# Optimization experiments

Measured on AMD Instinct MI355X. Metric: run time of the kernel, lower is better.

## Reference

```python
import jax, jax.numpy as jnp
import numpy as np

B, LIN, DIN, D, NQ, H, NB, DI, DS, K, DTR = 4, 2048, 512, 1024, 256, 16, 4, 2048, 16, 4, 64


def _ln(x, g, b, eps=1e-5):
    m = x.mean(-1, keepdims=True)
    v = ((x - m) ** 2).mean(-1, keepdims=True)
    return (x - m) * jax.lax.rsqrt(v + eps) * g + b


def setup_inputs() -> dict:
    key = jax.random.key(0)
    ks = iter(jax.random.split(key, 40))
    r = lambda *s: jax.random.normal(next(ks), s, jnp.float32) * 0.02
    inp = dict(
        x=jax.random.normal(next(ks), (B, LIN, DIN), jnp.float32),
        mask=jnp.ones((B, LIN), bool),
        W_in=r(D, DIN), b_in=jnp.zeros((D,), jnp.float32),
        latents=r(1, NQ, D),
        lnq_g=jnp.ones((D,), jnp.float32), lnq_b=jnp.zeros((D,), jnp.float32),
        lnkv_g=jnp.ones((D,), jnp.float32), lnkv_b=jnp.zeros((D,), jnp.float32),
        W_qkv=r(3 * D, D), b_qkv=jnp.zeros((3 * D,), jnp.float32),
        W_o=r(D, D), b_o=jnp.zeros((D,), jnp.float32),
        W1=r(2 * D, D), b1=jnp.zeros((2 * D,), jnp.float32),
        W2=r(D, 2 * D), b2=jnp.zeros((D,), jnp.float32),
        lnf_g=jnp.ones((D,), jnp.float32), lnf_b=jnp.zeros((D,), jnp.float32),
        mb_ln_g=jnp.ones((NB, D), jnp.float32), mb_ln_b=jnp.zeros((NB, D), jnp.float32),
        mb_Win=r(NB, 2 * DI, D),
        mb_conv_w=r(NB, DI, K), mb_conv_b=jnp.zeros((NB, DI), jnp.float32),
        mb_xproj=r(NB, DTR + 2 * DS, DI),
        mb_dtW=r(NB, DI, DTR), mb_dtb=r(NB, DI),
        mb_Alog=jnp.log(jnp.broadcast_to(jnp.arange(1, DS + 1, dtype=jnp.float32), (NB, DI, DS))),
        mb_D=jnp.ones((NB, DI), jnp.float32),
        mb_Wout=r(NB, D, DI),
        enc_ln_g=jnp.ones((D,), jnp.float32), enc_ln_b=jnp.zeros((D,), jnp.float32),
        out_ln_g=jnp.ones((D,), jnp.float32), out_ln_b=jnp.zeros((D,), jnp.float32),
    )
    return inp


def _mamba(u, Win, cw, cb, xp, dtW, dtb, Alog, Dp, Wout):
    # u: [B, NQ, D]
    xz = u @ Win.T                              # [B, NQ, 2*DI]
    xin, z = jnp.split(xz, 2, axis=-1)
    # causal depthwise conv1d over time
    xc = jax.lax.conv_general_dilated(
        xin.transpose(0, 2, 1), cw[:, None, :], (1,), [(K - 1, 0)],
        feature_group_count=DI)                 # [B, DI, NQ]
    xc = jax.nn.silu((xc + cb[None, :, None]).transpose(0, 2, 1))  # [B, NQ, DI]
    dbl = xc @ xp.T                             # [B, NQ, DTR + 2*DS]
    dtr = dbl[..., :DTR]
    Bm = dbl[..., DTR:DTR + DS]
    Cm = dbl[..., DTR + DS:]
    delta = jax.nn.softplus(dtr @ dtW.T + dtb)  # [B, NQ, DI]
    A = -jnp.exp(Alog)                          # [DI, DS]

    def step(h, inputs):
        dt, bt, ct, xt = inputs                 # dt,xt: [B,DI]; bt,ct: [B,DS]
        h = jnp.exp(dt[..., None] * A) * h + (dt * xt)[..., None] * bt[:, None, :]
        return h, jnp.einsum('bdn,bn->bd', h, ct)

    xs = (delta.transpose(1, 0, 2), Bm.transpose(1, 0, 2),
          Cm.transpose(1, 0, 2), xc.transpose(1, 0, 2))
    h0 = jnp.zeros((u.shape[0], DI, DS), u.dtype)
    _, ys = jax.lax.scan(step, h0, xs)          # ys: [NQ, B, DI]
    y = ys.transpose(1, 0, 2) + Dp * xc
    return (y * jax.nn.silu(z)) @ Wout.T


def reference(x, mask, W_in, b_in, latents, lnq_g, lnq_b, lnkv_g, lnkv_b,
              W_qkv, b_qkv, W_o, b_o, W1, b1, W2, b2, lnf_g, lnf_b,
              mb_ln_g, mb_ln_b, mb_Win, mb_conv_w, mb_conv_b, mb_xproj,
              mb_dtW, mb_dtb, mb_Alog, mb_D, mb_Wout,
              enc_ln_g, enc_ln_b, out_ln_g, out_ln_b):
    bsz = x.shape[0]
    h = x @ W_in.T + b_in                               # [B, LIN, D]
    q = _ln(jnp.broadcast_to(latents, (bsz, NQ, D)), lnq_g, lnq_b)
    kv = _ln(h, lnkv_g, lnkv_b)
    Wq, Wk, Wv = jnp.split(W_qkv, 3, 0)
    bq, bk, bv = jnp.split(b_qkv, 3, 0)
    hd = D // H
    qh = (q @ Wq.T + bq).reshape(bsz, NQ, H, hd)
    kh = (kv @ Wk.T + bk).reshape(bsz, LIN, H, hd)
    vh = (kv @ Wv.T + bv).reshape(bsz, LIN, H, hd)
    sc = jnp.einsum('bqhd,bkhd->bhqk', qh, kh) / jnp.float32(np.sqrt(hd))
    sc = jnp.where(mask[:, None, None, :], sc, jnp.float32(-1e9))
    attn = jax.nn.softmax(sc, axis=-1)
    o = jnp.einsum('bhqk,bkhd->bqhd', attn, vh).reshape(bsz, NQ, D) @ W_o.T + b_o
    hq = q + o
    ff = jax.nn.gelu(hq @ W1.T + b1, approximate=False) @ W2.T + b2
    hq = _ln(hq + ff, lnf_g, lnf_b)
    for i in range(mb_ln_g.shape[0]):
        hq = hq + _mamba(_ln(hq, mb_ln_g[i], mb_ln_b[i]), mb_Win[i],
                         mb_conv_w[i], mb_conv_b[i], mb_xproj[i], mb_dtW[i],
                         mb_dtb[i], mb_Alog[i], mb_D[i], mb_Wout[i])
    hq = _ln(hq, enc_ln_g, enc_ln_b)
    out = _ln(hq, out_ln_g, out_ln_b)
    comp_mask = jnp.ones((bsz, NQ), bool)
    return (out, comp_mask)
```

## Files before the change

kernel.cpp:

```cpp
#include <hip/hip_runtime.h>
#include <hip/hip_bf16.h>
#include <math.h>

typedef __attribute__((ext_vector_type(8))) short s16x8;
typedef __attribute__((ext_vector_type(4))) float f32x4;

static __device__ __forceinline__ unsigned short f2bf(float f) {
    unsigned u = __builtin_bit_cast(unsigned, f);
    u += 0x7fffu + ((u >> 16) & 1u);
    return (unsigned short)(u >> 16);
}

static __device__ __forceinline__ void gload16(const void* g, void* l) {
    __builtin_amdgcn_global_load_lds(
        (const __attribute__((address_space(1))) unsigned int*)g,
        (__attribute__((address_space(3))) unsigned int*)l, 16, 0, 0);
}

template<int ACT, bool ACC, bool BIAS, int OUT>
__global__ __launch_bounds__(256)
void gemm_bf16(const unsigned short* __restrict__ A, const unsigned short* __restrict__ B,
               const float* __restrict__ bias, float* __restrict__ Cf,
               unsigned short* __restrict__ Cb,
               int M, int N, int K, int lda, int ldb, int ldc)
{
    __shared__ alignas(16) unsigned short As[128][32];
    __shared__ alignas(16) unsigned short Bs[128][32];

    const int tid = threadIdx.x;
    const int m0 = blockIdx.y * 128;
    const int n0 = blockIdx.x * 128;
    const int l  = tid & 63;
    const int w  = tid >> 6;
    const int wr = w >> 1, wc = w & 1;
    const int fr = l & 15;
    const int fk = (l >> 4) * 8;
    const int srow = l >> 2;
    const int skel = (l & 3) * 8;

    f32x4 acc[4][4];
#pragma unroll
    for (int i = 0; i < 4; ++i)
#pragma unroll
        for (int j = 0; j < 4; ++j) acc[i][j] = (f32x4){0.f, 0.f, 0.f, 0.f};

    for (int k0 = 0; k0 < K; k0 += 32) {
#pragma unroll
        for (int c = 0; c < 2; ++c) {
            const int r0 = w * 32 + c * 16;
            gload16(A + (size_t)(m0 + r0 + srow) * lda + k0 + skel, &As[r0][0]);
            gload16(B + (size_t)(n0 + r0 + srow) * ldb + k0 + skel, &Bs[r0][0]);
        }
        __syncthreads();

        s16x8 af[4], bfg[4];
#pragma unroll
        for (int mi = 0; mi < 4; ++mi)
            af[mi] = *reinterpret_cast<const s16x8*>(&As[wr * 64 + mi * 16 + fr][fk]);
#pragma unroll
        for (int ni = 0; ni < 4; ++ni)
            bfg[ni] = *reinterpret_cast<const s16x8*>(&Bs[wc * 64 + ni * 16 + fr][fk]);
#pragma unroll
        for (int mi = 0; mi < 4; ++mi)
#pragma unroll
            for (int ni = 0; ni < 4; ++ni)
                acc[mi][ni] = __builtin_amdgcn_mfma_f32_16x16x32_bf16(
                    af[mi], bfg[ni], acc[mi][ni], 0, 0, 0);
        __syncthreads();
    }

#pragma unroll
    for (int mi = 0; mi < 4; ++mi) {
#pragma unroll
        for (int ni = 0; ni < 4; ++ni) {
            const int col = n0 + wc * 64 + ni * 16 + fr;
            float bs = BIAS ? bias[col] : 0.f;
            f32x4 v = acc[mi][ni];
#pragma unroll
            for (int r = 0; r < 4; ++r) {
                const int row = m0 + wr * 64 + mi * 16 + (l >> 4) * 4 + r;
                float val = v[r] + bs;
                if (ACT == 1) val = 0.5f * val * (1.0f + erff(val * 0.70710678118654752440f));
                size_t idx = (size_t)row * ldc + col;
                if (OUT == 0) {
                    if (ACC) val += Cf[idx];
                    Cf[idx] = val;
                } else {
                    Cb[idx] = f2bf(val);
                }
            }
        }
    }
}

template<int ACT, bool ACC, bool BIAS, int OUT>
__global__ __launch_bounds__(256)
void gemm_bf16_t64(const unsigned short* __restrict__ A, const unsigned short* __restrict__ B,
                   const float* __restrict__ bias, float* __restrict__ Cf,
                   unsigned short* __restrict__ Cb,
                   int M, int N, int K, int lda, int ldb, int ldc)
{
    __shared__ alignas(16) unsigned short As[64][32];
    __shared__ alignas(16) unsigned short Bs[64][32];

    const int tid = threadIdx.x;
    const int m0 = blockIdx.y * 64;
    const int n0 = blockIdx.x * 64;
    const int l  = tid & 63;
    const int w  = tid >> 6;
    const int wr = w >> 1, wc = w & 1;
    const int fr = l & 15;
    const int fk = (l >> 4) * 8;

    f32x4 acc[2][2];
#pragma unroll
    for (int i = 0; i < 2; ++i)
#pragma unroll
        for (int j = 0; j < 2; ++j) acc[i][j] = (f32x4){0.f, 0.f, 0.f, 0.f};

    for (int k0 = 0; k0 < K; k0 += 32) {
        gload16(A + (size_t)(m0 + w * 16 + (l >> 2)) * lda + k0 + (l & 3) * 8, &As[w * 16][0]);
        gload16(B + (size_t)(n0 + w * 16 + (l >> 2)) * ldb + k0 + (l & 3) * 8, &Bs[w * 16][0]);
        __syncthreads();

        s16x8 af[2], bfg[2];
#pragma unroll
        for (int mi = 0; mi < 2; ++mi)
            af[mi] = *reinterpret_cast<const s16x8*>(&As[wr * 32 + mi * 16 + fr][fk]);
#pragma unroll
        for (int ni = 0; ni < 2; ++ni)
            bfg[ni] = *reinterpret_cast<const s16x8*>(&Bs[wc * 32 + ni * 16 + fr][fk]);
#pragma unroll
        for (int mi = 0; mi < 2; ++mi)
#pragma unroll
            for (int ni = 0; ni < 2; ++ni)
                acc[mi][ni] = __builtin_amdgcn_mfma_f32_16x16x32_bf16(
                    af[mi], bfg[ni], acc[mi][ni], 0, 0, 0);
        __syncthreads();
    }

#pragma unroll
    for (int mi = 0; mi < 2; ++mi) {
#pragma unroll
        for (int ni = 0; ni < 2; ++ni) {
            const int col = n0 + wc * 32 + ni * 16 + fr;
            float bs = BIAS ? bias[col] : 0.f;
            f32x4 v = acc[mi][ni];
#pragma unroll
            for (int r = 0; r < 4; ++r) {
                const int row = m0 + wr * 32 + mi * 16 + (l >> 4) * 4 + r;
                float val = v[r] + bs;
                if (ACT == 1) val = 0.5f * val * (1.0f + erff(val * 0.70710678118654752440f));
                size_t idx = (size_t)row * ldc + col;
                if (OUT == 0) {
                    if (ACC) val += Cf[idx];
                    Cf[idx] = val;
                } else {
                    Cb[idx] = f2bf(val);
                }
            }
        }
    }
}

template<int ACT, bool BIAS, bool ATOMIC>
__global__ __launch_bounds__(256)
void gemm_bt(const float* __restrict__ A, const float* __restrict__ B,
             const float* __restrict__ bias, float* __restrict__ C,
             int M, int N, int K, int lda, int ldb, int ldc, int ksplit)
{
    __shared__ alignas(16) float As[16][68];
    __shared__ alignas(16) float Bs[16][68];
    const int tid = threadIdx.x;
    const int m0 = blockIdx.y * 64;
    const int n0 = blockIdx.x * 64;
    const int ty = tid >> 4, tx = tid & 15;
    const int lrow = tid >> 2;
    const int lk   = (tid & 3) << 2;

    float acc[4][4] = {};
    const int kbeg = blockIdx.z * ksplit;
    const int kend = kbeg + ksplit;

    for (int k0 = kbeg; k0 < kend; k0 += 16) {
        {
            int gr = m0 + lrow;
            float4 v; v.x = v.y = v.z = v.w = 0.f;
            if (gr < M) v = *reinterpret_cast<const float4*>(A + (size_t)gr * lda + k0 + lk);
            As[lk + 0][lrow] = v.x; As[lk + 1][lrow] = v.y;
            As[lk + 2][lrow] = v.z; As[lk + 3][lrow] = v.w;
        }
        {
            int gr = n0 + lrow;
            float4 v; v.x = v.y = v.z = v.w = 0.f;
            if (gr < N) v = *reinterpret_cast<const float4*>(B + (size_t)gr * ldb + k0 + lk);
            Bs[lk + 0][lrow] = v.x; Bs[lk + 1][lrow] = v.y;
            Bs[lk + 2][lrow] = v.z; Bs[lk + 3][lrow] = v.w;
        }
        __syncthreads();
#pragma unroll
        for (int k = 0; k < 16; ++k) {
            float4 a = *reinterpret_cast<const float4*>(&As[k][ty << 2]);
            float4 b = *reinterpret_cast<const float4*>(&Bs[k][tx << 2]);
            acc[0][0] += a.x * b.x; acc[0][1] += a.x * b.y; acc[0][2] += a.x * b.z; acc[0][3] += a.x * b.w;
            acc[1][0] += a.y * b.x; acc[1][1] += a.y * b.y; acc[1][2] += a.y * b.z; acc[1][3] += a.y * b.w;
            acc[2][0] += a.z * b.x; acc[2][1] += a.z * b.y; acc[2][2] += a.z * b.z; acc[2][3] += a.z * b.w;
            acc[3][0] += a.w * b.x; acc[3][1] += a.w * b.y; acc[3][2] += a.w * b.z; acc[3][3] += a.w * b.w;
        }
        __syncthreads();
    }

#pragma unroll
    for (int i = 0; i < 4; ++i) {
        int m = m0 + (ty << 2) + i;
        if (m >= M) continue;
#pragma unroll
        for (int j = 0; j < 4; ++j) {
            int n = n0 + (tx << 2) + j;
            if (n >= N) continue;
            float v = acc[i][j];
            if (BIAS && blockIdx.z == 0) v += bias[n];
            if (ACT == 2) v = fmaxf(v, 0.f) + log1pf(expf(-fabsf(v)));
            size_t idx = (size_t)m * ldc + n;
            if (ATOMIC) atomicAdd(&C[idx], v);
            else C[idx] = v;
        }
    }
}

template<bool RES, int OUT>
__global__ __launch_bounds__(256)
void ln_k(const float* __restrict__ x, const float* __restrict__ res,
          const float* __restrict__ g, const float* __restrict__ b,
          float* __restrict__ outf, unsigned short* __restrict__ outb)
{
    int row = blockIdx.x;
    int t = threadIdx.x;
    float4 v = reinterpret_cast<const float4*>(x + (size_t)row * 1024)[t];
    if (RES) {
        float4 r2 = reinterpret_cast<const float4*>(res + (size_t)row * 1024)[t];
        v.x += r2.x; v.y += r2.y; v.z += r2.z; v.w += r2.w;
    }
    float s  = v.x + v.y + v.z + v.w;
    float ss = v.x * v.x + v.y * v.y + v.z * v.z + v.w * v.w;
#pragma unroll
    for (int off = 32; off > 0; off >>= 1) {
        s  += __shfl_down(s, off, 64);
        ss += __shfl_down(ss, off, 64);
    }
    __shared__ float red[2][4];
    __shared__ float mv[2];
    int wid = t >> 6;
    if ((t & 63) == 0) { red[0][wid] = s; red[1][wid] = ss; }
    __syncthreads();
    if (t == 0) {
        float S  = red[0][0] + red[0][1] + red[0][2] + red[0][3];
        float SS = red[1][0] + red[1][1] + red[1][2] + red[1][3];
        float mean = S * (1.f / 1024.f);
        float var  = SS * (1.f / 1024.f) - mean * mean;
        mv[0] = mean; mv[1] = rsqrtf(var + 1e-5f);
    }
    __syncthreads();
    float mean = mv[0], rstd = mv[1];
    float4 gg = reinterpret_cast<const float4*>(g)[t];
    float4 bb = reinterpret_cast<const float4*>(b)[t];
    float y0 = (v.x - mean) * rstd * gg.x + bb.x;
    float y1 = (v.y - mean) * rstd * gg.y + bb.y;
    float y2 = (v.z - mean) * rstd * gg.z + bb.z;
    float y3 = (v.w - mean) * rstd * gg.w + bb.w;
    if (OUT == 0 || OUT == 2) {
        float4 ov; ov.x = y0; ov.y = y1; ov.z = y2; ov.w = y3;
        reinterpret_cast<float4*>(outf + (size_t)row * 1024)[t] = ov;
    }
    if (OUT == 1 || OUT == 2) {
        unsigned long long p = (unsigned long long)f2bf(y0)
                             | ((unsigned long long)f2bf(y1) << 16)
                             | ((unsigned long long)f2bf(y2) << 32)
                             | ((unsigned long long)f2bf(y3) << 48);
        *reinterpret_cast<unsigned long long*>(outb + (size_t)row * 1024 + t * 4) = p;
    }
}

__global__ __launch_bounds__(256)
void attn_part_mfma(const unsigned short* __restrict__ qh,
                    const unsigned short* __restrict__ kv,
                    float* __restrict__ pacc, float* __restrict__ pml)
{
    const int bx = blockIdx.x;
    const int split = bx & 3;
    const int qsp = (bx >> 2) & 3;
    const int h = (bx >> 4) & 15;
    const int b = bx >> 8;
    const int tid = threadIdx.x;
    const int l = tid & 63, w = tid >> 6;
    const int g = l >> 4, q4 = l & 15;

    __shared__ alignas(16) unsigned short Ks[64][72];
    __shared__ alignas(16) unsigned short Vt[64][72];
    __shared__ alignas(16) unsigned short Ps[4][64][20];

    s16x8 qf[2];
    {
        const int qrow = qsp * 64 + w * 16 + q4;
        const unsigned short* qp = qh + (size_t)qrow * 1024 + h * 64 + g * 8;
        qf[0] = *reinterpret_cast<const s16x8*>(qp);
        qf[1] = *reinterpret_cast<const s16x8*>(qp + 32);
    }

    f32x4 oacc[4];
#pragma unroll
    for (int mi = 0; mi < 4; ++mi) oacc[mi] = (f32x4){0.f, 0.f, 0.f, 0.f};
    float m_run = -1e30f, l_run = 0.f;

    const unsigned short* khb = kv + ((size_t)b * 2048 + split * 512) * 2048 + h * 64;
    const unsigned short* vhb = khb + 1024;

    const int krow = tid >> 2, dcol = (tid & 3) << 4;

    for (int kt = 0; kt < 512; kt += 64) {
        __syncthreads();
        {
            const unsigned short* ksrc = khb + (size_t)(kt + krow) * 2048 + dcol;
            s16x8 k0 = *reinterpret_cast<const s16x8*>(ksrc);
            s16x8 k1 = *reinterpret_cast<const s16x8*>(ksrc + 8);
            *reinterpret_cast<s16x8*>(&Ks[krow][dcol]) = k0;
            *reinterpret_cast<s16x8*>(&Ks[krow][dcol + 8]) = k1;
            const unsigned short* vsrc = vhb + (size_t)(kt + krow) * 2048 + dcol;
            s16x8 v0 = *reinterpret_cast<const s16x8*>(vsrc);
            s16x8 v1 = *reinterpret_cast<const s16x8*>(vsrc + 8);
            const int kb = krow >> 3, klo = krow & 7;
#pragma unroll
            for (int ii = 0; ii < 8; ++ii) {
                int d0 = dcol + ii, d1 = dcol + 8 + ii;
                Vt[d0][((kb ^ ((d0 >> 3) & 7)) << 3) + klo] = (unsigned short)v0[ii];
                Vt[d1][((kb ^ ((d1 >> 3) & 7)) << 3) + klo] = (unsigned short)v1[ii];
            }
        }
        __syncthreads();

        f32x4 sacc[4];
#pragma unroll
        for (int mt = 0; mt < 4; ++mt) sacc[mt] = (f32x4){0.f, 0.f, 0.f, 0.f};
#pragma unroll
        for (int dc = 0; dc < 2; ++dc) {
#pragma unroll
            for (int mt = 0; mt < 4; ++mt) {
                s16x8 ka = *reinterpret_cast<const s16x8*>(&Ks[mt * 16 + q4][g * 8 + dc * 32]);
                sacc[mt] = __builtin_amdgcn_mfma_f32_16x16x32_bf16(ka, qf[dc], sacc[mt], 0, 0, 0);
            }
        }

        float p[16];
        float pmax = -1e30f;
#pragma unroll
        for (int mt = 0; mt < 4; ++mt)
#pragma unroll
            for (int r = 0; r < 4; ++r)
                pmax = fmaxf(pmax, sacc[mt][r] * 0.125f);
        pmax = fmaxf(pmax, __shfl_xor(pmax, 16));
        pmax = fmaxf(pmax, __shfl_xor(pmax, 32));
        float m_new = fmaxf(m_run, pmax);
        float sc_o = __expf(m_run - m_new);
        float lpart = 0.f;
#pragma unroll
        for (int mt = 0; mt < 4; ++mt)
#pragma unroll
            for (int r = 0; r < 4; ++r) {
                float pv = __expf(sacc[mt][r] * 0.125f - m_new);
                p[mt * 4 + r] = pv;
                lpart += pv;
            }
        lpart += __shfl_xor(lpart, 16);
        lpart += __shfl_xor(lpart, 32);
        l_run = l_run * sc_o + lpart;
        m_run = m_new;
#pragma unroll
        for (int mi = 0; mi < 4; ++mi)
#pragma unroll
            for (int r = 0; r < 4; ++r)
                oacc[mi][r] *= sc_o;

#pragma unroll
        for (int mt = 0; mt < 4; ++mt)
#pragma unroll
            for (int r = 0; r < 4; ++r)
                Ps[w][mt * 16 + g * 4 + r][q4] = f2bf(p[mt * 4 + r]);

#pragma unroll
        for (int kc = 0; kc < 2; ++kc) {
            s16x8 pb;
#pragma unroll
            for (int j = 0; j < 8; ++j)
                pb[j] = (short)Ps[w][kc * 32 + g * 8 + j][q4];
#pragma unroll
            for (int mi = 0; mi < 4; ++mi) {
                const int d = mi * 16 + q4;
                s16x8 va = *reinterpret_cast<const s16x8*>(
                    &Vt[d][((4 * kc + g) ^ ((d >> 3) & 7)) << 3]);
                oacc[mi] = __builtin_amdgcn_mfma_f32_16x16x32_bf16(va, pb, oacc[mi], 0, 0, 0);
            }
        }
    }

    const int rowg = (b * 16 + h) * 256 + qsp * 64 + w * 16 + q4;
    float* pa = pacc + ((size_t)split * 16384 + rowg) * 64;
#pragma unroll
    for (int mi = 0; mi < 4; ++mi)
        *reinterpret_cast<f32x4*>(pa + mi * 16 + g * 4) = oacc[mi];
    if (g == 0) {
        pml[((size_t)split * 16384 + rowg) * 2 + 0] = m_run;
        pml[((size_t)split * 16384 + rowg) * 2 + 1] = l_run;
    }
}

__global__ __launch_bounds__(64)
void attn_comb_k(const float* __restrict__ pacc, const float* __restrict__ pml,
                 unsigned short* __restrict__ o)
{
    int row = blockIdx.x * 64 + threadIdx.x;
    float M = -1e30f;
#pragma unroll
    for (int s = 0; s < 4; ++s)
        M = fmaxf(M, pml[((size_t)s * 16384 + row) * 2]);
    float L = 0.f;
    float out[64] = {};
#pragma unroll
    for (int s = 0; s < 4; ++s) {
        float ms = pml[((size_t)s * 16384 + row) * 2 + 0];
        float ls = pml[((size_t)s * 16384 + row) * 2 + 1];
        float wgt = __expf(ms - M);
        L += wgt * ls;
        const float4* ap = reinterpret_cast<const float4*>(pacc + ((size_t)s * 16384 + row) * 64);
#pragma unroll
        for (int d4 = 0; d4 < 16; ++d4) {
            float4 a = ap[d4];
            out[d4 * 4 + 0] += wgt * a.x; out[d4 * 4 + 1] += wgt * a.y;
            out[d4 * 4 + 2] += wgt * a.z; out[d4 * 4 + 3] += wgt * a.w;
        }
    }
    float inv = 1.f / L;
    int t = row & 63, qt = (row >> 6) & 3, h = (row >> 8) & 15, b = row >> 12;
    unsigned short* op = o + (size_t)(b * 256 + qt * 64 + t) * 1024 + h * 64;
#pragma unroll
    for (int d8 = 0; d8 < 8; ++d8) {
        s16x8 v;
#pragma unroll
        for (int j = 0; j < 8; ++j) v[j] = (short)f2bf(out[d8 * 8 + j] * inv);
        *reinterpret_cast<s16x8*>(op + d8 * 8) = v;
    }
}

__global__ void add_bcast_k(const float* __restrict__ q, const float* __restrict__ o,
                            float* __restrict__ hq, unsigned short* __restrict__ hqb)
{
    int i = blockIdx.x * 256 + threadIdx.x;
    int r = i >> 8, c = i & 255;
    float4 qv = reinterpret_cast<const float4*>(q)[(r & 255) * 256 + c];
    float4 ov = reinterpret_cast<const float4*>(o)[i];
    float4 s; s.x = qv.x + ov.x; s.y = qv.y + ov.y; s.z = qv.z + ov.z; s.w = qv.w + ov.w;
    reinterpret_cast<float4*>(hq)[i] = s;
    unsigned long long p = (unsigned long long)f2bf(s.x)
                         | ((unsigned long long)f2bf(s.y) << 16)
                         | ((unsigned long long)f2bf(s.z) << 32)
                         | ((unsigned long long)f2bf(s.w) << 48);
    *reinterpret_cast<unsigned long long*>(hqb + (size_t)r * 1024 + c * 4) = p;
}

__global__ void conv_k(const float* __restrict__ xz, const float* __restrict__ cw,
                       const float* __restrict__ cb, float* __restrict__ xc)
{
    int i = blockIdx.x * 256 + threadIdx.x;
    int r = i >> 11, c = i & 2047;
    int t = r & 255;
    float a = cb[c];
#pragma unroll
    for (int k = 0; k < 4; ++k) {
        int tt = t - 3 + k;
        if (tt >= 0) a += xz[(size_t)(r - 3 + k) * 4096 + c] * cw[c * 4 + k];
    }
    xc[i] = a / (1.f + expf(-a));
}

__global__ __launch_bounds__(256)
void scan_gate_k(const float* __restrict__ delta, const float* __restrict__ dbl,
                 const float* __restrict__ xc, const float* __restrict__ Alog,
                 const float* __restrict__ xz, const float* __restrict__ Dp,
                 unsigned short* __restrict__ gb)
{
    const int t = threadIdx.x;
    const int pi = t & 15, seg = t >> 4;
    const int pr = blockIdx.x * 16 + pi;
    const int c = pr & 2047, b = pr >> 11;

    float A[16];
#pragma unroll
    for (int n = 0; n < 16; ++n) A[n] = -expf(Alog[c * 16 + n]);
    const float Dc = Dp[c];

    __shared__ float HE[15][16][17];
    __shared__ float HU[15][16][17];

    if (seg < 15) {
        float h[16], E[16];
#pragma unroll
        for (int n = 0; n < 16; ++n) { h[n] = 0.f; E[n] = 1.f; }
        for (int s = 0; s < 16; ++s) {
            int r = b * 256 + seg * 16 + s;
            float dt = delta[(size_t)r * 2048 + c];
            float xv = xc[(size_t)r * 2048 + c];
            const float* row = dbl + (size_t)r * 96;
            float dx = dt * xv;
#pragma unroll
            for (int n = 0; n < 16; ++n) {
                float e = __expf(dt * A[n]);
                h[n] = e * h[n] + dx * row[64 + n];
                E[n] *= e;
            }
        }
#pragma unroll
        for (int n = 0; n < 16; ++n) { HE[seg][pi][n] = E[n]; HU[seg][pi][n] = h[n]; }
    }
    __syncthreads();

    float hs[16];
#pragma unroll
    for (int n = 0; n < 16; ++n) hs[n] = 0.f;
    for (int s2 = 0; s2 < seg; ++s2) {
#pragma unroll
        for (int n = 0; n < 16; ++n)
            hs[n] = HE[s2][pi][n] * hs[n] + HU[s2][pi][n];
    }

    for (int s = 0; s < 16; ++s) {
        int r = b * 256 + seg * 16 + s;
        float dt = delta[(size_t)r * 2048 + c];
        float xv = xc[(size_t)r * 2048 + c];
        const float* row = dbl + (size_t)r * 96;
        float dx = dt * xv;
        float y = 0.f;
#pragma unroll
        for (int n = 0; n < 16; ++n) {
            float e = __expf(dt * A[n]);
            hs[n] = e * hs[n] + dx * row[64 + n];
            y += hs[n] * row[80 + n];
        }
        float zv = xz[(size_t)r * 4096 + 2048 + c];
        float gv = (y + Dc * xv) * (zv / (1.f + expf(-zv)));
        gb[(size_t)r * 2048 + c] = f2bf(gv);
    }
}

__global__ __launch_bounds__(256)
void cvt_bf16_k(const float* __restrict__ in, unsigned short* __restrict__ out)
{
    size_t i = ((size_t)blockIdx.x * 256 + threadIdx.x) * 8;
    float4 a = *reinterpret_cast<const float4*>(in + i);
    float4 b = *reinterpret_cast<const float4*>(in + i + 4);
    s16x8 v;
    v[0] = (short)f2bf(a.x); v[1] = (short)f2bf(a.y);
    v[2] = (short)f2bf(a.z); v[3] = (short)f2bf(a.w);
    v[4] = (short)f2bf(b.x); v[5] = (short)f2bf(b.y);
    v[6] = (short)f2bf(b.z); v[7] = (short)f2bf(b.w);
    *reinterpret_cast<s16x8*>(out + i) = v;
}

__global__ void fill_ones_f32(float* p, int n)
{
    int i = blockIdx.x * 256 + threadIdx.x;
    if (i < n) p[i] = 1.0f;
}

__global__ void fill_zero_f32(float* p, int n)
{
    int i = blockIdx.x * 256 + threadIdx.x;
    if (i < n) p[i] = 0.0f;
}

extern "C" void kernel_launch(void* const* d_in, const int* in_sizes, int n_in,
                              void* d_out, int out_size, void* d_ws, size_t ws_size,
                              hipStream_t stream)
{
    const float* x      = (const float*)d_in[0];
    const float* W_in   = (const float*)d_in[2];
    const float* b_in   = (const float*)d_in[3];
    const float* latents= (const float*)d_in[4];
    const float* lnq_g  = (const float*)d_in[5];
    const float* lnq_b  = (const float*)d_in[6];
    const float* lnkv_g = (const float*)d_in[7];
    const float* lnkv_b = (const float*)d_in[8];
    const float* W_qkv  = (const float*)d_in[9];
    const float* b_qkv  = (const float*)d_in[10];
    const float* W_o    = (const float*)d_in[11];
    const float* b_o    = (const float*)d_in[12];
    const float* W1     = (const float*)d_in[13];
    const float* b1     = (const float*)d_in[14];
    const float* W2     = (const float*)d_in[15];
    const float* b2     = (const float*)d_in[16];
    const float* lnf_g  = (const float*)d_in[17];
    const float* lnf_b  = (const float*)d_in[18];
    const float* mb_ln_g= (const float*)d_in[19];
    const float* mb_ln_b= (const float*)d_in[20];
    const float* mb_Win = (const float*)d_in[21];
    const float* mb_cw  = (const float*)d_in[22];
    const float* mb_cb  = (const float*)d_in[23];
    const float* mb_xp  = (const float*)d_in[24];
    const float* mb_dtW = (const float*)d_in[25];
    const float* mb_dtb = (const float*)d_in[26];
    const float* mb_Alog= (const float*)d_in[27];
    const float* mb_D   = (const float*)d_in[28];
    const float* mb_Wout= (const float*)d_in[29];
    const float* enc_g  = (const float*)d_in[30];
    const float* enc_b  = (const float*)d_in[31];
    const float* out_g  = (const float*)d_in[32];
    const float* out_b  = (const float*)d_in[33];

    float* W = (float*)d_ws;
    typedef unsigned short us;
    float* kvh  = W + 0;
    float* qln  = W + 25165824;
    float* op   = W + 26738688;
    float* hq   = W + 27787264;
    us* P       = (us*)(W + 8388608);
    us* kv_bf   = P + 0;
    us* KV      = P + 8388608;
    us* qh_bf   = P + 25165824;
    us* Wqkv_bf = P + 25427968;
    us* Win_bf  = P + 28573696;
    us* xbf     = P + 29097984;
    float* pacc = kvh;
    float* pml  = op;
    us* Wo_bf   = (us*)(W + 4194304);
    us* W1_bf   = (us*)(W + 4718592);
    us* W2_bf   = (us*)(W + 5767168);
    us* ff1_bf  = (us*)(W + 6815744);
    us* hq_bf   = (us*)(W + 7864320);
    us* o_bf    = (us*)(W + 25690112);
    us* qln_bf  = (us*)(W + 26214400);
    us* Win_all = (us*)(W + 8388608);
    us* Wout_all= (us*)(W + 16777216);
    us* u_bf    = (us*)(W + 0);
    float* xz   = W + 524288;
    float* xc   = W + 4718592;
    float* dbl  = W + 6815744;
    float* dly  = W + 20971520;
    us* gb_bf   = (us*)(W + 23068672);
    float* tmp  = W + 26214400;

    dim3 blk(256);

    cvt_bf16_k<<<2048,blk,0,stream>>>(x, xbf);
    cvt_bf16_k<<<256,blk,0,stream>>>(W_in, Win_bf);
    cvt_bf16_k<<<1536,blk,0,stream>>>(W_qkv, Wqkv_bf);
    gemm_bf16<0,false,true,0><<<dim3(8,64),blk,0,stream>>>(xbf, Win_bf, b_in, kvh, nullptr, 8192,1024,512, 512,512,1024);
    ln_k<false,1><<<8192,blk,0,stream>>>(kvh, nullptr, lnkv_g, lnkv_b, nullptr, kv_bf);
    ln_k<false,2><<<256,blk,0,stream>>>(latents, nullptr, lnq_g, lnq_b, qln, qln_bf);
    gemm_bf16_t64<0,false,true,1><<<dim3(16,4),blk,0,stream>>>(qln_bf, Wqkv_bf, b_qkv, nullptr, qh_bf, 256,1024,1024, 1024,1024,1024);
    gemm_bf16<0,false,true,1><<<dim3(16,64),blk,0,stream>>>(kv_bf, Wqkv_bf+1048576, b_qkv+1024, nullptr, KV, 8192,2048,1024, 1024,1024,2048);
    attn_part_mfma<<<1024,blk,0,stream>>>(qh_bf, KV, pacc, pml);
    cvt_bf16_k<<<512,blk,0,stream>>>(W_o, Wo_bf);
    attn_comb_k<<<256,64,0,stream>>>(pacc, pml, o_bf);
    gemm_bf16_t64<0,false,true,0><<<dim3(16,16),blk,0,stream>>>(o_bf, Wo_bf, b_o, op, nullptr, 1024,1024,1024, 1024,1024,1024);
    add_bcast_k<<<1024,blk,0,stream>>>(qln, op, hq, hq_bf);
    cvt_bf16_k<<<1024,blk,0,stream>>>(W1, W1_bf);
    cvt_bf16_k<<<1024,blk,0,stream>>>(W2, W2_bf);
    gemm_bf16_t64<1,false,true,1><<<dim3(32,16),blk,0,stream>>>(hq_bf, W1_bf, b1, nullptr, ff1_bf, 1024,2048,1024, 1024,1024,2048);
    gemm_bf16_t64<0,false,true,0><<<dim3(16,16),blk,0,stream>>>(ff1_bf, W2_bf, b2, tmp, nullptr, 1024,1024,2048, 2048,2048,1024);
    ln_k<true,0><<<1024,blk,0,stream>>>(hq, tmp, lnf_g, lnf_b, hq, nullptr);
    cvt_bf16_k<<<8192,blk,0,stream>>>(mb_Win, Win_all);
    cvt_bf16_k<<<4096,blk,0,stream>>>(mb_Wout, Wout_all);
    for (int i = 0; i < 4; ++i) {
        ln_k<false,1><<<1024,blk,0,stream>>>(hq, nullptr, mb_ln_g + i*1024, mb_ln_b + i*1024, nullptr, u_bf);
        gemm_bf16<0,false,false,0><<<dim3(32,8),blk,0,stream>>>(u_bf, Win_all + (size_t)i*4194304, nullptr, xz, nullptr, 1024,4096,1024, 1024,1024,4096);
        conv_k<<<8192,blk,0,stream>>>(xz, mb_cw + i*8192, mb_cb + i*2048, xc);
        fill_zero_f32<<<384,blk,0,stream>>>(dbl, 98304);
        gemm_bt<0,false,true><<<dim3(2,16,8),blk,0,stream>>>(xc, mb_xp + i*196608, nullptr, dbl, 1024,96,2048, 2048,2048,96, 256);
        gemm_bt<2,true,false><<<dim3(32,16,1),blk,0,stream>>>(dbl, mb_dtW + i*131072, mb_dtb + i*2048, dly, 1024,2048,64, 96,64,2048, 64);
        scan_gate_k<<<512,blk,0,stream>>>(dly, dbl, xc, mb_Alog + i*32768, xz, mb_D + i*2048, gb_bf);
        gemm_bf16_t64<0,true,false,0><<<dim3(16,16),blk,0,stream>>>(gb_bf, Wout_all + (size_t)i*2097152, nullptr, hq, nullptr, 1024,1024,2048, 2048,2048,1024);
    }
    ln_k<false,0><<<1024,blk,0,stream>>>(hq, nullptr, enc_g, enc_b, tmp, nullptr);
    ln_k<false,0><<<1024,blk,0,stream>>>(tmp, nullptr, out_g, out_b, (float*)d_out, nullptr);
    fill_ones_f32<<<4,blk,0,stream>>>((float*)d_out + 1048576, 1024);
}
```

Before: 1.015 ms.

## Add 256x256-tile GEMM for KV projection and batch weight conversions into multi-kernels

Adds a 512-thread GEMM kernel with 256x256 output tiles and a 64-wide K step, and uses it for the large 8192x2048x1024 KV projection to raise data reuse per block. It also merges eight separate fp32-to-bf16 conversion launches into two multi-segment launches, so fewer kernels are launched. The big tile uses 64KB of LDS and 128 accumulator registers per thread, with no double buffering. That can lower occupancy, and the grid has only 256 blocks.

```diff
diff --git a/kernel.cpp b/kernel.cpp
--- a/kernel.cpp
+++ b/kernel.cpp
@@ -93,6 +93,78 @@
     }
 }
 
+template<bool BIAS, int OUT>
+__global__ __launch_bounds__(512)
+void gemm_bf16_t256(const unsigned short* __restrict__ A, const unsigned short* __restrict__ B,
+                    const float* __restrict__ bias, float* __restrict__ Cf,
+                    unsigned short* __restrict__ Cb,
+                    int M, int N, int K, int lda, int ldb, int ldc)
+{
+    __shared__ alignas(16) unsigned short As[256][64];
+    __shared__ alignas(16) unsigned short Bs[256][64];
+
+    const int tid = threadIdx.x;
+    const int m0 = blockIdx.y * 256;
+    const int n0 = blockIdx.x * 256;
+    const int l  = tid & 63;
+    const int w  = tid >> 6;
+    const int wr = w >> 2, wc = w & 3;
+    const int fr = l & 15;
+    const int fk = (l >> 4) * 8;
+
+    f32x4 acc[8][4];
+#pragma unroll
+    for (int i = 0; i < 8; ++i)
+#pragma unroll
+        for (int j = 0; j < 4; ++j) acc[i][j] = (f32x4){0.f, 0.f, 0.f, 0.f};
+
+    for (int k0 = 0; k0 < K; k0 += 64) {
+#pragma unroll
+        for (int c = 0; c < 4; ++c) {
+            const int r0 = (w * 4 + c) * 8;
+            gload16(A + (size_t)(m0 + r0 + (l >> 3)) * lda + k0 + (l & 7) * 8, &As[r0][0]);
+            gload16(B + (size_t)(n0 + r0 + (l >> 3)) * ldb + k0 + (l & 7) * 8, &Bs[r0][0]);
+        }
+        __syncthreads();
+
+#pragma unroll
+        for (int kk = 0; kk < 2; ++kk) {
+            s16x8 af[8], bfg[4];
+#pragma unroll
+            for (int mi = 0; mi < 8; ++mi)
+                af[mi] = *reinterpret_cast<const s16x8*>(&As[wr * 128 + mi * 16 + fr][kk * 32 + fk]);
+#pragma unroll
+            for (int ni = 0; ni < 4; ++ni)
+                bfg[ni] = *reinterpret_cast<const s16x8*>(&Bs[wc * 64 + ni * 16 + fr][kk * 32 + fk]);
+#pragma unroll
+            for (int mi = 0; mi < 8; ++mi)
+#pragma unroll
+                for (int ni = 0; ni < 4; ++ni)
+                    acc[mi][ni] = __builtin_amdgcn_mfma_f32_16x16x32_bf16(
+                        af[mi], bfg[ni], acc[mi][ni], 0, 0, 0);
+        }
+        __syncthreads();
+    }
+
+#pragma unroll
+    for (int mi = 0; mi < 8; ++mi) {
+#pragma unroll
+        for (int ni = 0; ni < 4; ++ni) {
+            const int col = n0 + wc * 64 + ni * 16 + fr;
+            float bs = BIAS ? bias[col] : 0.f;
+            f32x4 v = acc[mi][ni];
+#pragma unroll
+            for (int r = 0; r < 4; ++r) {
+                const int row = m0 + wr * 128 + mi * 16 + (l >> 4) * 4 + r;
+                float val = v[r] + bs;
+                size_t idx = (size_t)row * ldc + col;
+                if (OUT == 0) Cf[idx] = val;
+                else          Cb[idx] = f2bf(val);
+            }
+        }
+    }
+}
+
 template<int ACT, bool ACC, bool BIAS, int OUT>
 __global__ __launch_bounds__(256)
 void gemm_bf16_t64(const unsigned short* __restrict__ A, const unsigned short* __restrict__ B,
@@ -551,17 +623,28 @@
 }
 
 __global__ __launch_bounds__(256)
-void cvt_bf16_k(const float* __restrict__ in, unsigned short* __restrict__ out)
-{
-    size_t i = ((size_t)blockIdx.x * 256 + threadIdx.x) * 8;
-    float4 a = *reinterpret_cast<const float4*>(in + i);
-    float4 b = *reinterpret_cast<const float4*>(in + i + 4);
+void cvt_multi_k(const float* s0, const float* s1, const float* s2,
+                 const float* s3, const float* s4,
+                 unsigned short* d0, unsigned short* d1, unsigned short* d2,
+                 unsigned short* d3, unsigned short* d4,
+                 int e0, int e1, int e2, int e3, int e4)
+{
+    int blk = blockIdx.x;
+    const float* s; unsigned short* d; int base;
+    if      (blk < e0) { s = s0; d = d0; base = 0;  }
+    else if (blk < e1) { s = s1; d = d1; base = e0; }
+    else if (blk < e2) { s = s2; d = d2; base = e1; }
+    else if (blk < e3) { s = s3; d = d3; base = e2; }
+    else               { s = s4; d = d4; base = e3; }
+    size_t i = ((size_t)(blk - base) * 256 + threadIdx.x) * 8;
+    float4 a = *reinterpret_cast<const float4*>(s + i);
+    float4 b = *reinterpret_cast<const float4*>(s + i + 4);
     s16x8 v;
     v[0] = (short)f2bf(a.x); v[1] = (short)f2bf(a.y);
     v[2] = (short)f2bf(a.z); v[3] = (short)f2bf(a.w);
     v[4] = (short)f2bf(b.x); v[5] = (short)f2bf(b.y);
     v[6] = (short)f2bf(b.z); v[7] = (short)f2bf(b.w);
-    *reinterpret_cast<s16x8*>(out + i) = v;
+    *reinterpret_cast<s16x8*>(d + i) = v;
 }
 
 __global__ void fill_ones_f32(float* p, int n)
@@ -648,26 +731,24 @@
 
     dim3 blk(256);
 
-    cvt_bf16_k<<<2048,blk,0,stream>>>(x, xbf);
-    cvt_bf16_k<<<256,blk,0,stream>>>(W_in, Win_bf);
-    cvt_bf16_k<<<1536,blk,0,stream>>>(W_qkv, Wqkv_bf);
+    cvt_multi_k<<<3840,blk,0,stream>>>(x, W_in, W_qkv, W_qkv, W_qkv,
+                                       xbf, Win_bf, Wqkv_bf, Wqkv_bf, Wqkv_bf,
+                                       2048, 2304, 3840, 3840, 3840);
     gemm_bf16<0,false,true,0><<<dim3(8,64),blk,0,stream>>>(xbf, Win_bf, b_in, kvh, nullptr, 8192,1024,512, 512,512,1024);
     ln_k<false,1><<<8192,blk,0,stream>>>(kvh, nullptr, lnkv_g, lnkv_b, nullptr, kv_bf);
     ln_k<false,2><<<256,blk,0,stream>>>(latents, nullptr, lnq_g, lnq_b, qln, qln_bf);
     gemm_bf16_t64<0,false,true,1><<<dim3(16,4),blk,0,stream>>>(qln_bf, Wqkv_bf, b_qkv, nullptr, qh_bf, 256,1024,1024, 1024,1024,1024);
-    gemm_bf16<0,false,true,1><<<dim3(16,64),blk,0,stream>>>(kv_bf, Wqkv_bf+1048576, b_qkv+1024, nullptr, KV, 8192,2048,1024, 1024,1024,2048);
+    gemm_bf16_t256<true,1><<<dim3(8,32),dim3(512),0,stream>>>(kv_bf, Wqkv_bf+1048576, b_qkv+1024, nullptr, KV, 8192,2048,1024, 1024,1024,2048);
     attn_part_mfma<<<1024,blk,0,stream>>>(qh_bf, KV, pacc, pml);
-    cvt_bf16_k<<<512,blk,0,stream>>>(W_o, Wo_bf);
     attn_comb_k<<<256,64,0,stream>>>(pacc, pml, o_bf);
+    cvt_multi_k<<<14848,blk,0,stream>>>(W_o, W1, W2, mb_Win, mb_Wout,
+                                        Wo_bf, W1_bf, W2_bf, Win_all, Wout_all,
+                                        512, 1536, 2560, 10752, 14848);
     gemm_bf16_t64<0,false,true,0><<<dim3(16,16),blk,0,stream>>>(o_bf, Wo_bf, b_o, op, nullptr, 1024,1024,1024, 1024,1024,1024);
     add_bcast_k<<<1024,blk,0,stream>>>(qln, op, hq, hq_bf);
-    cvt_bf16_k<<<1024,blk,0,stream>>>(W1, W1_bf);
-    cvt_bf16_k<<<1024,blk,0,stream>>>(W2, W2_bf);
     gemm_bf16_t64<1,false,true,1><<<dim3(32,16),blk,0,stream>>>(hq_bf, W1_bf, b1, nullptr, ff1_bf, 1024,2048,1024, 1024,1024,2048);
     gemm_bf16_t64<0,false,true,0><<<dim3(16,16),blk,0,stream>>>(ff1_bf, W2_bf, b2, tmp, nullptr, 1024,1024,2048, 2048,2048,1024);
     ln_k<true,0><<<1024,blk,0,stream>>>(hq, tmp, lnf_g, lnf_b, hq, nullptr);
-    cvt_bf16_k<<<8192,blk,0,stream>>>(mb_Win, Win_all);
-    cvt_bf16_k<<<4096,blk,0,stream>>>(mb_Wout, Wout_all);
     for (int i = 0; i < 4; ++i) {
         ln_k<false,1><<<1024,blk,0,stream>>>(hq, nullptr, mb_ln_g + i*1024, mb_ln_b + i*1024, nullptr, u_bf);
         gemm_bf16<0,false,false,0><<<dim3(32,8),blk,0,stream>>>(u_bf, Win_all + (size_t)i*4194304, nullptr, xz, nullptr, 1024,4096,1024, 1024,1024,4096);
```

Result: no change. 1.022 ms (+0.8%).
